# Kernel optimization log

Measured on AMD Instinct MI355X. Metric: run time of the kernel, lower is better.

Reference implementation:

```python
import jax, jax.numpy as jnp
import numpy as np

B, NQ, C = 2, 10000, 256
M, L, K = 8, 3, 4
D = C // M
LEVEL_SHAPES = [(100, 100), (50, 50), (25, 25)]


def setup_inputs() -> dict:
    key = jax.random.key(0)
    ks = jax.random.split(key, 16)
    inp = {
        "query": jax.random.normal(ks[0], (B, NQ, C), jnp.float32),
        "reference_points": jax.random.uniform(ks[1], (B, NQ, 2), jnp.float32),
        "value0": jax.random.normal(ks[2], (B, C) + LEVEL_SHAPES[0], jnp.float32),
        "value1": jax.random.normal(ks[3], (B, C) + LEVEL_SHAPES[1], jnp.float32),
        "value2": jax.random.normal(ks[4], (B, C) + LEVEL_SHAPES[2], jnp.float32),
        "Wv": jax.random.normal(ks[5], (C, C), jnp.float32) * 0.02,
        "bv": jnp.zeros((C,), jnp.float32),
        "Ws": jax.random.normal(ks[6], (M * L * K * 2, C), jnp.float32) * 0.05,
        "bs": jax.random.normal(ks[7], (M * L * K * 2,), jnp.float32),
        "Wa": jax.random.normal(ks[8], (M * L * K, C), jnp.float32) * 0.02,
        "ba": jnp.zeros((M * L * K,), jnp.float32),
        "Wo": jax.random.normal(ks[9], (C, C), jnp.float32) * 0.02,
        "bo": jnp.zeros((C,), jnp.float32),
    }
    return inp


def _bilinear_sample(vflat, px, py, H, W):
    """grid_sample bilinear, align_corners=False, padding_mode='zeros'.
    vflat: (B, M, H*W, D); px, py: (B, M, Q, K) pixel coords. -> (B, M, Q, K, D)
    """
    b, m, q, k = px.shape
    x0 = jnp.floor(px)
    y0 = jnp.floor(py)
    wx1 = px - x0  # frac weights (grad 1 w.r.t. px, matching grid_sample)
    wy1 = py - y0
    wx0 = 1.0 - wx1
    wy0 = 1.0 - wy1

    def gather(xi, yi):
        valid = ((xi >= 0) & (xi <= W - 1) & (yi >= 0) & (yi <= H - 1)).astype(vflat.dtype)
        xc = jnp.clip(xi, 0, W - 1).astype(jnp.int32)
        yc = jnp.clip(yi, 0, H - 1).astype(jnp.int32)
        idx = (yc * W + xc).reshape(b, m, q * k)
        g = jnp.take_along_axis(vflat, idx[..., None], axis=2)  # (B,M,QK,D)
        return g.reshape(b, m, q, k, -1) * valid[..., None]

    out = (gather(x0, y0) * (wx0 * wy0)[..., None]
           + gather(x0 + 1, y0) * (wx1 * wy0)[..., None]
           + gather(x0, y0 + 1) * (wx0 * wy1)[..., None]
           + gather(x0 + 1, y0 + 1) * (wx1 * wy1)[..., None])
    return out


def reference(query, reference_points, value0, value1, value2,
              Wv, bv, Ws, bs, Wa, ba, Wo, bo):
    bsz, nq, c = query.shape
    dt = query.dtype
    # sampling offsets and attention weights
    off = (query @ Ws.T + bs).reshape(bsz, nq, M, L, K, 2)
    attn = jax.nn.softmax((query @ Wa.T + ba).reshape(bsz, nq, M, L * K), axis=-1)
    attn = attn.reshape(bsz, nq, M, L, K)

    out = jnp.zeros((bsz, nq, M, D), dt)
    for li, v in enumerate([value0, value1, value2]):
        H, W = v.shape[2], v.shape[3]
        # conv1x1 value projection -> per-head maps (B, M, H*W, D)
        proj = jnp.einsum('bchw,oc->bohw', v, Wv) + bv[None, :, None, None]
        vflat = proj.reshape(bsz, M, D, H * W).transpose(0, 1, 3, 2)
        norm = jnp.asarray([W, H], dt)
        loc = reference_points[:, :, None, None, :] + off[:, :, :, li, :, :] / norm  # (B,Q,M,K,2)
        # grid = loc*2-1; pixel = (grid+1)*size/2 - 0.5 = loc*size - 0.5
        px = (loc[..., 0] * W - 0.5).transpose(0, 2, 1, 3)  # (B,M,Q,K)
        py = (loc[..., 1] * H - 0.5).transpose(0, 2, 1, 3)
        sampled = _bilinear_sample(vflat, px, py, H, W)  # (B,M,Q,K,D)
        out = out + jnp.einsum('bmqkd,bqmk->bqmd', sampled, attn[:, :, :, li, :])

    out = out.reshape(bsz, nq, c)
    return out @ Wo.T + bo
```

## Files before the change

### kernel.cpp

```cpp
#include <hip/hip_runtime.h>
#include <cstddef>

#define B_ 2
#define NQ_ 10000
#define C_ 256
#define M_ 8
#define L_ 3
#define K_ 4
#define D_ 32
#define P_ 13125

typedef unsigned short u16;
typedef __attribute__((ext_vector_type(8))) short short8;
typedef __attribute__((ext_vector_type(4))) float f32x4;

static __device__ __forceinline__ u16 f2bf(float f) {
    union { float f; unsigned u; } x; x.f = f;
    unsigned r = x.u + 0x7fffu + ((x.u >> 16) & 1u);
    return (u16)(r >> 16);
}
static __device__ __forceinline__ float bf2f(u16 u) {
    union { unsigned u; float f; } x; x.u = (unsigned)u << 16;
    return x.f;
}
static __device__ __forceinline__ short8 cvt8(const float4& a, const float4& b) {
    short8 r;
    r[0] = (short)f2bf(a.x); r[1] = (short)f2bf(a.y);
    r[2] = (short)f2bf(a.z); r[3] = (short)f2bf(a.w);
    r[4] = (short)f2bf(b.x); r[5] = (short)f2bf(b.y);
    r[6] = (short)f2bf(b.z); r[7] = (short)f2bf(b.w);
    return r;
}

__global__ __launch_bounds__(256) void transpose_value(
    const float* __restrict__ v0, const float* __restrict__ v1,
    const float* __restrict__ v2, u16* __restrict__ Vt)
{
    constexpr int HWs[3]  = {10000, 2500, 625};
    constexpr int offs[3] = {0, 10000, 12500};

    const int z   = blockIdx.z;
    const int b   = z / 3;
    const int lvl = z % 3;
    const int HW  = HWs[lvl];
    const int p0  = blockIdx.x * 64;
    if (p0 >= HW) return;
    const int c0  = blockIdx.y * 64;

    const float* V = (lvl == 0 ? v0 : (lvl == 1 ? v1 : v2)) + (size_t)b * 256 * HW;

    __shared__ u16 tile[64][66];
    const int t  = threadIdx.x;
    const int pl = t & 63;
    const int cb = t >> 6;

    #pragma unroll
    for (int i = 0; i < 16; ++i) {
        int c = cb + i * 4;
        float vv = 0.f;
        if (p0 + pl < HW)
            vv = V[(size_t)(c0 + c) * HW + p0 + pl];
        tile[pl][c] = f2bf(vv);
    }
    __syncthreads();

    const int cl = t & 63;
    const int pb = t >> 6;
    #pragma unroll
    for (int i = 0; i < 16; ++i) {
        int p = pb + i * 4;
        if (p0 + p < HW)
            Vt[((size_t)b * P_ + offs[lvl] + p0 + p) * 256 + c0 + cl] = tile[p][cl];
    }
}

template <bool AF32, typename OutT>
__global__ __launch_bounds__(256) void gemm_panel(
    const void* __restrict__ Av, int rows, int nRowTiles, int npanel,
    const float* __restrict__ B1f, const float* __restrict__ bias1, int N1,
    const float* __restrict__ B2f, const float* __restrict__ bias2, int Ntot,
    OutT* __restrict__ Cout)
{
    __shared__ u16 Bs[64 * 264];

    const int bid  = blockIdx.x;
    const int rlo  = bid & 7;
    const int tmp  = bid >> 3;
    const int panel = tmp % npanel;
    const int rowTile = (tmp / npanel) * 8 + rlo;
    if (rowTile >= nRowTiles) return;

    const int t  = threadIdx.x;
    const int w  = t >> 6;
    const int l  = t & 63;
    const int row0 = rowTile * 128 + w * 32;
    const int o0   = panel * 64;
    const int lr = l & 15;
    const int kb = (l >> 4) * 8;

    #pragma unroll
    for (int i = 0; i < 8; ++i) {
        int idx = i * 256 + t;
        int col = idx >> 5;
        int kc  = (idx & 31) * 8;
        int colg = min(o0 + col, Ntot - 1);
        const float* Br = ((colg < N1) ? B1f + (size_t)colg * 256
                                       : B2f + (size_t)(colg - N1) * 256) + kc;
        float4 f0 = *reinterpret_cast<const float4*>(Br);
        float4 f1 = *reinterpret_cast<const float4*>(Br + 4);
        *reinterpret_cast<short8*>(&Bs[col * 264 + kc]) = cvt8(f0, f1);
    }

    const int ra0 = min(row0 + lr,      rows - 1);
    const int ra1 = min(row0 + 16 + lr, rows - 1);

    __syncthreads();

    f32x4 acc[2][4] = {};

    if constexpr (AF32) {
        const float* Af  = (const float*)Av;
        const float* Ap0 = Af + (size_t)ra0 * 256 + kb;
        const float* Ap1 = Af + (size_t)ra1 * 256 + kb;
        #pragma unroll
        for (int k0 = 0; k0 < 256; k0 += 32) {
            float4 x0 = *reinterpret_cast<const float4*>(Ap0 + k0);
            float4 y0 = *reinterpret_cast<const float4*>(Ap0 + k0 + 4);
            float4 x1 = *reinterpret_cast<const float4*>(Ap1 + k0);
            float4 y1 = *reinterpret_cast<const float4*>(Ap1 + k0 + 4);
            short8 a0 = cvt8(x0, y0);
            short8 a1 = cvt8(x1, y1);
            short8 b0 = *reinterpret_cast<const short8*>(&Bs[(0 * 16 + lr) * 264 + kb + k0]);
            short8 b1 = *reinterpret_cast<const short8*>(&Bs[(1 * 16 + lr) * 264 + kb + k0]);
            short8 b2 = *reinterpret_cast<const short8*>(&Bs[(2 * 16 + lr) * 264 + kb + k0]);
            short8 b3 = *reinterpret_cast<const short8*>(&Bs[(3 * 16 + lr) * 264 + kb + k0]);
            acc[0][0] = __builtin_amdgcn_mfma_f32_16x16x32_bf16(a0, b0, acc[0][0], 0, 0, 0);
            acc[0][1] = __builtin_amdgcn_mfma_f32_16x16x32_bf16(a0, b1, acc[0][1], 0, 0, 0);
            acc[0][2] = __builtin_amdgcn_mfma_f32_16x16x32_bf16(a0, b2, acc[0][2], 0, 0, 0);
            acc[0][3] = __builtin_amdgcn_mfma_f32_16x16x32_bf16(a0, b3, acc[0][3], 0, 0, 0);
            acc[1][0] = __builtin_amdgcn_mfma_f32_16x16x32_bf16(a1, b0, acc[1][0], 0, 0, 0);
            acc[1][1] = __builtin_amdgcn_mfma_f32_16x16x32_bf16(a1, b1, acc[1][1], 0, 0, 0);
            acc[1][2] = __builtin_amdgcn_mfma_f32_16x16x32_bf16(a1, b2, acc[1][2], 0, 0, 0);
            acc[1][3] = __builtin_amdgcn_mfma_f32_16x16x32_bf16(a1, b3, acc[1][3], 0, 0, 0);
        }
    } else {
        const u16* Af  = (const u16*)Av;
        const u16* Ap0 = Af + (size_t)ra0 * 256 + kb;
        const u16* Ap1 = Af + (size_t)ra1 * 256 + kb;
        #pragma unroll
        for (int k0 = 0; k0 < 256; k0 += 32) {
            short8 a0 = *reinterpret_cast<const short8*>(Ap0 + k0);
            short8 a1 = *reinterpret_cast<const short8*>(Ap1 + k0);
            short8 b0 = *reinterpret_cast<const short8*>(&Bs[(0 * 16 + lr) * 264 + kb + k0]);
            short8 b1 = *reinterpret_cast<const short8*>(&Bs[(1 * 16 + lr) * 264 + kb + k0]);
            short8 b2 = *reinterpret_cast<const short8*>(&Bs[(2 * 16 + lr) * 264 + kb + k0]);
            short8 b3 = *reinterpret_cast<const short8*>(&Bs[(3 * 16 + lr) * 264 + kb + k0]);
            acc[0][0] = __builtin_amdgcn_mfma_f32_16x16x32_bf16(a0, b0, acc[0][0], 0, 0, 0);
            acc[0][1] = __builtin_amdgcn_mfma_f32_16x16x32_bf16(a0, b1, acc[0][1], 0, 0, 0);
            acc[0][2] = __builtin_amdgcn_mfma_f32_16x16x32_bf16(a0, b2, acc[0][2], 0, 0, 0);
            acc[0][3] = __builtin_amdgcn_mfma_f32_16x16x32_bf16(a0, b3, acc[0][3], 0, 0, 0);
            acc[1][0] = __builtin_amdgcn_mfma_f32_16x16x32_bf16(a1, b0, acc[1][0], 0, 0, 0);
            acc[1][1] = __builtin_amdgcn_mfma_f32_16x16x32_bf16(a1, b1, acc[1][1], 0, 0, 0);
            acc[1][2] = __builtin_amdgcn_mfma_f32_16x16x32_bf16(a1, b2, acc[1][2], 0, 0, 0);
            acc[1][3] = __builtin_amdgcn_mfma_f32_16x16x32_bf16(a1, b3, acc[1][3], 0, 0, 0);
        }
    }

    const int orow = (l >> 4) * 4;
    #pragma unroll
    for (int ct = 0; ct < 4; ++ct) {
        const int col = o0 + ct * 16 + lr;
        if (col >= Ntot) continue;
        const float bsv = (col < N1) ? bias1[col] : bias2[col - N1];
        #pragma unroll
        for (int rt = 0; rt < 2; ++rt) {
            #pragma unroll
            for (int r = 0; r < 4; ++r) {
                const int row = row0 + rt * 16 + orow + r;
                if (row < rows) {
                    float val = acc[rt][ct][r] + bsv;
                    if constexpr (sizeof(OutT) == 2)
                        Cout[(size_t)row * Ntot + col] = (OutT)f2bf(val);
                    else
                        Cout[(size_t)row * Ntot + col] = (OutT)val;
                }
            }
        }
    }
}

__global__ __launch_bounds__(256) void sample_kernel(
    const float* __restrict__ S,
    const float* __restrict__ refp,
    const u16* __restrict__ proj,
    u16* __restrict__ out2)
{
    constexpr int Wd[3]   = {100, 50, 25};
    constexpr int offs[3] = {0, 10000, 12500};

    __shared__ int   midx[192][4];
    __shared__ float mw[192][4];

    const int t = threadIdx.x;

    if (t < 192) {
        const int q  = t / 96;
        const int tq = t % 96;
        const int tm = tq / 12;
        const int tj = tq % 12;
        const int bq = blockIdx.x * 2 + q;
        const float* Sq = S + (size_t)bq * 288;

        float lg[12], mx = -1e30f;
        #pragma unroll
        for (int jj = 0; jj < 12; ++jj) {
            lg[jj] = Sq[192 + tm * 12 + jj];
            mx = fmaxf(mx, lg[jj]);
        }
        float sum = 0.f;
        #pragma unroll
        for (int jj = 0; jj < 12; ++jj) sum += __expf(lg[jj] - mx);
        const float attn = __expf(lg[tj] - mx) / sum;

        const int l  = tj >> 2;
        const int Wl = Wd[l];
        const float refx = refp[(size_t)bq * 2 + 0];
        const float refy = refp[(size_t)bq * 2 + 1];
        const float ox = Sq[(tm * 12 + tj) * 2 + 0];
        const float oy = Sq[(tm * 12 + tj) * 2 + 1];
        const float px = refx * (float)Wl + ox - 0.5f;
        const float py = refy * (float)Wl + oy - 0.5f;
        const float x0f = floorf(px), y0f = floorf(py);
        const float wx1 = px - x0f, wy1 = py - y0f;
        const float wx0 = 1.f - wx1, wy0 = 1.f - wy1;
        const int x0 = (int)x0f, y0 = (int)y0f;
        const int x1 = x0 + 1, y1 = y0 + 1;
        const bool vx0 = (unsigned)x0 < (unsigned)Wl;
        const bool vx1 = (unsigned)x1 < (unsigned)Wl;
        const bool vy0 = (unsigned)y0 < (unsigned)Wl;
        const bool vy1 = (unsigned)y1 < (unsigned)Wl;
        const int chb  = tm * 32;
        const int base = offs[l];
        midx[t][0] = (vx0 && vy0) ? ((base + y0 * Wl + x0) * 256 + chb) : 0;
        midx[t][1] = (vx1 && vy0) ? ((base + y0 * Wl + x1) * 256 + chb) : 0;
        midx[t][2] = (vx0 && vy1) ? ((base + y1 * Wl + x0) * 256 + chb) : 0;
        midx[t][3] = (vx1 && vy1) ? ((base + y1 * Wl + x1) * 256 + chb) : 0;
        mw[t][0] = (vx0 && vy0) ? attn * wx0 * wy0 : 0.f;
        mw[t][1] = (vx1 && vy0) ? attn * wx1 * wy0 : 0.f;
        mw[t][2] = (vx0 && vy1) ? attn * wx0 * wy1 : 0.f;
        mw[t][3] = (vx1 && vy1) ? attn * wx1 * wy1 : 0.f;
    }
    __syncthreads();

    const int qi  = t >> 7;
    const int tt  = t & 127;
    const int mh  = tt >> 4;
    const int d16 = tt & 15;
    const int bq2 = blockIdx.x * 2 + qi;
    const int b   = bq2 / NQ_;
    const u16* projb = proj + (size_t)b * P_ * 256 + 2 * d16;

    float acc0 = 0.f, acc1 = 0.f;

    #pragma unroll
    for (int j = 0; j < 12; ++j) {
        const int mj = qi * 96 + mh * 12 + j;
        const int4   o  = *reinterpret_cast<const int4*>(midx[mj]);
        const float4 ww = *reinterpret_cast<const float4*>(mw[mj]);
        const unsigned u00 = *reinterpret_cast<const unsigned*>(projb + o.x);
        const unsigned u10 = *reinterpret_cast<const unsigned*>(projb + o.y);
        const unsigned u01 = *reinterpret_cast<const unsigned*>(projb + o.z);
        const unsigned u11 = *reinterpret_cast<const unsigned*>(projb + o.w);
        union { unsigned u; float f; } c0, c1;
        c0.u = u00 << 16;          c1.u = u00 & 0xffff0000u;
        acc0 = fmaf(ww.x, c0.f, acc0); acc1 = fmaf(ww.x, c1.f, acc1);
        c0.u = u10 << 16;          c1.u = u10 & 0xffff0000u;
        acc0 = fmaf(ww.y, c0.f, acc0); acc1 = fmaf(ww.y, c1.f, acc1);
        c0.u = u01 << 16;          c1.u = u01 & 0xffff0000u;
        acc0 = fmaf(ww.z, c0.f, acc0); acc1 = fmaf(ww.z, c1.f, acc1);
        c0.u = u11 << 16;          c1.u = u11 & 0xffff0000u;
        acc0 = fmaf(ww.w, c0.f, acc0); acc1 = fmaf(ww.w, c1.f, acc1);
    }

    const unsigned packed = (unsigned)f2bf(acc0) | ((unsigned)f2bf(acc1) << 16);
    *reinterpret_cast<unsigned*>(out2 + (size_t)bq2 * 256 + mh * 32 + 2 * d16) = packed;
}

extern "C" void kernel_launch(void* const* d_in, const int* in_sizes, int n_in,
                              void* d_out, int out_size, void* d_ws, size_t ws_size,
                              hipStream_t stream)
{
    const float* query = (const float*)d_in[0];
    const float* refp  = (const float*)d_in[1];
    const float* v0    = (const float*)d_in[2];
    const float* v1    = (const float*)d_in[3];
    const float* v2    = (const float*)d_in[4];
    const float* Wv    = (const float*)d_in[5];
    const float* bv    = (const float*)d_in[6];
    const float* Ws    = (const float*)d_in[7];
    const float* bs    = (const float*)d_in[8];
    const float* Wa    = (const float*)d_in[9];
    const float* ba    = (const float*)d_in[10];
    const float* Wo    = (const float*)d_in[11];
    const float* bo    = (const float*)d_in[12];
    float* out = (float*)d_out;

    char* wsb = (char*)d_ws;
    u16*   proj  = (u16*)wsb;    wsb += (size_t)B_ * P_ * 256 * 2;
    float* S     = (float*)wsb;  wsb += (size_t)B_ * NQ_ * 288 * 4;
    u16*   Vt    = (u16*)wsb;    wsb += (size_t)B_ * P_ * 256 * 2;
    u16*   out2  = (u16*)wsb;    wsb += (size_t)B_ * NQ_ * 256 * 2;

    dim3 blk(256);

    transpose_value<<<dim3(157, 4, 6), blk, 0, stream>>>(v0, v1, v2, Vt);

    gemm_panel<false, u16><<<dim3(832), blk, 0, stream>>>(
        Vt, B_ * P_, 206, 4, Wv, bv, 256, Wv, bv, 256, proj);

    gemm_panel<true, float><<<dim3(800), blk, 0, stream>>>(
        query, B_ * NQ_, 157, 5, Ws, bs, 192, Wa, ba, 288, S);

    sample_kernel<<<dim3(NQ_), blk, 0, stream>>>(S, refp, proj, out2);

    gemm_panel<false, float><<<dim3(640), blk, 0, stream>>>(
        out2, B_ * NQ_, 157, 4, Wo, bo, 256, Wo, bo, 256, out);
}
```

Before: 202.5 us.

## Pre-convert query to bf16 and widen sampling kernel to four queries per block

Adds a standalone kernel that converts the fp32 query to bf16, so the offset/attention GEMM reads bf16 input instead of converting fp32 on the fly. The sampling kernel now handles four queries per block, with each thread loading four bf16 channels (8 bytes) per corner instead of two. It also software-pipelines the corner loads three steps ahead. This adds an extra kernel launch and a round trip of the query through memory, and increases register pressure in the sampler.

```diff
diff --git a/kernel.cpp b/kernel.cpp
--- a/kernel.cpp
+++ b/kernel.cpp
@@ -19,10 +19,6 @@
     unsigned r = x.u + 0x7fffu + ((x.u >> 16) & 1u);
     return (u16)(r >> 16);
 }
-static __device__ __forceinline__ float bf2f(u16 u) {
-    union { unsigned u; float f; } x; x.u = (unsigned)u << 16;
-    return x.f;
-}
 static __device__ __forceinline__ short8 cvt8(const float4& a, const float4& b) {
     short8 r;
     r[0] = (short)f2bf(a.x); r[1] = (short)f2bf(a.y);
@@ -30,6 +26,16 @@
     r[4] = (short)f2bf(b.x); r[5] = (short)f2bf(b.y);
     r[6] = (short)f2bf(b.z); r[7] = (short)f2bf(b.w);
     return r;
+}
+
+__global__ __launch_bounds__(256) void cvt_f32_bf16(
+    const float* __restrict__ in, u16* __restrict__ out, int n8)
+{
+    const int i = blockIdx.x * 256 + threadIdx.x;
+    if (i >= n8) return;
+    const float4 a = *reinterpret_cast<const float4*>(in + (size_t)i * 8);
+    const float4 b = *reinterpret_cast<const float4*>(in + (size_t)i * 8 + 4);
+    *reinterpret_cast<short8*>(out + (size_t)i * 8) = cvt8(a, b);
 }
 
 __global__ __launch_bounds__(256) void transpose_value(
@@ -198,17 +204,17 @@
     constexpr int Wd[3]   = {100, 50, 25};
     constexpr int offs[3] = {0, 10000, 12500};
 
-    __shared__ int   midx[192][4];
-    __shared__ float mw[192][4];
+    __shared__ int   midx[384][4];
+    __shared__ float mw[384][4];
 
     const int t = threadIdx.x;
 
-    if (t < 192) {
-        const int q  = t / 96;
-        const int tq = t % 96;
+    for (int job = t; job < 384; job += 256) {
+        const int q  = job / 96;
+        const int tq = job % 96;
         const int tm = tq / 12;
         const int tj = tq % 12;
-        const int bq = blockIdx.x * 2 + q;
+        const int bq = blockIdx.x * 4 + q;
         const float* Sq = S + (size_t)bq * 288;
 
         float lg[12], mx = -1e30f;
@@ -241,49 +247,71 @@
         const bool vy1 = (unsigned)y1 < (unsigned)Wl;
         const int chb  = tm * 32;
         const int base = offs[l];
-        midx[t][0] = (vx0 && vy0) ? ((base + y0 * Wl + x0) * 256 + chb) : 0;
-        midx[t][1] = (vx1 && vy0) ? ((base + y0 * Wl + x1) * 256 + chb) : 0;
-        midx[t][2] = (vx0 && vy1) ? ((base + y1 * Wl + x0) * 256 + chb) : 0;
-        midx[t][3] = (vx1 && vy1) ? ((base + y1 * Wl + x1) * 256 + chb) : 0;
-        mw[t][0] = (vx0 && vy0) ? attn * wx0 * wy0 : 0.f;
-        mw[t][1] = (vx1 && vy0) ? attn * wx1 * wy0 : 0.f;
-        mw[t][2] = (vx0 && vy1) ? attn * wx0 * wy1 : 0.f;
-        mw[t][3] = (vx1 && vy1) ? attn * wx1 * wy1 : 0.f;
+        midx[job][0] = (vx0 && vy0) ? ((base + y0 * Wl + x0) * 256 + chb) : 0;
+        midx[job][1] = (vx1 && vy0) ? ((base + y0 * Wl + x1) * 256 + chb) : 0;
+        midx[job][2] = (vx0 && vy1) ? ((base + y1 * Wl + x0) * 256 + chb) : 0;
+        midx[job][3] = (vx1 && vy1) ? ((base + y1 * Wl + x1) * 256 + chb) : 0;
+        mw[job][0] = (vx0 && vy0) ? attn * wx0 * wy0 : 0.f;
+        mw[job][1] = (vx1 && vy0) ? attn * wx1 * wy0 : 0.f;
+        mw[job][2] = (vx0 && vy1) ? attn * wx0 * wy1 : 0.f;
+        mw[job][3] = (vx1 && vy1) ? attn * wx1 * wy1 : 0.f;
     }
     __syncthreads();
 
-    const int qi  = t >> 7;
-    const int tt  = t & 127;
-    const int mh  = tt >> 4;
-    const int d16 = tt & 15;
-    const int bq2 = blockIdx.x * 2 + qi;
+    const int qi  = t >> 6;
+    const int tt  = t & 63;
+    const int mh  = tt >> 3;
+    const int d8  = tt & 7;
+    const int bq2 = blockIdx.x * 4 + qi;
     const int b   = bq2 / NQ_;
-    const u16* projb = proj + (size_t)b * P_ * 256 + 2 * d16;
-
-    float acc0 = 0.f, acc1 = 0.f;
+    const u16* projb = proj + (size_t)b * P_ * 256 + 4 * d8;
+    const int base_mj = qi * 96 + mh * 12;
+
+    float acc0 = 0.f, acc1 = 0.f, acc2 = 0.f, acc3 = 0.f;
+
+    uint2 v[4][4];
+    int4  o_[4];
+
+    #pragma unroll
+    for (int js = 0; js < 3; ++js) {
+        o_[js] = *reinterpret_cast<const int4*>(midx[base_mj + js]);
+        v[js][0] = *reinterpret_cast<const uint2*>(projb + o_[js].x);
+        v[js][1] = *reinterpret_cast<const uint2*>(projb + o_[js].y);
+        v[js][2] = *reinterpret_cast<const uint2*>(projb + o_[js].z);
+        v[js][3] = *reinterpret_cast<const uint2*>(projb + o_[js].w);
+    }
 
     #pragma unroll
     for (int j = 0; j < 12; ++j) {
-        const int mj = qi * 96 + mh * 12 + j;
-        const int4   o  = *reinterpret_cast<const int4*>(midx[mj]);
-        const float4 ww = *reinterpret_cast<const float4*>(mw[mj]);
-        const unsigned u00 = *reinterpret_cast<const unsigned*>(projb + o.x);
-        const unsigned u10 = *reinterpret_cast<const unsigned*>(projb + o.y);
-        const unsigned u01 = *reinterpret_cast<const unsigned*>(projb + o.z);
-        const unsigned u11 = *reinterpret_cast<const unsigned*>(projb + o.w);
-        union { unsigned u; float f; } c0, c1;
-        c0.u = u00 << 16;          c1.u = u00 & 0xffff0000u;
-        acc0 = fmaf(ww.x, c0.f, acc0); acc1 = fmaf(ww.x, c1.f, acc1);
-        c0.u = u10 << 16;          c1.u = u10 & 0xffff0000u;
-        acc0 = fmaf(ww.y, c0.f, acc0); acc1 = fmaf(ww.y, c1.f, acc1);
-        c0.u = u01 << 16;          c1.u = u01 & 0xffff0000u;
-        acc0 = fmaf(ww.z, c0.f, acc0); acc1 = fmaf(ww.z, c1.f, acc1);
-        c0.u = u11 << 16;          c1.u = u11 & 0xffff0000u;
-        acc0 = fmaf(ww.w, c0.f, acc0); acc1 = fmaf(ww.w, c1.f, acc1);
-    }
-
-    const unsigned packed = (unsigned)f2bf(acc0) | ((unsigned)f2bf(acc1) << 16);
-    *reinterpret_cast<unsigned*>(out2 + (size_t)bq2 * 256 + mh * 32 + 2 * d16) = packed;
+        const int s = j & 3;
+        if (j + 3 < 12) {
+            const int s3 = (j + 3) & 3;
+            o_[s3] = *reinterpret_cast<const int4*>(midx[base_mj + j + 3]);
+            v[s3][0] = *reinterpret_cast<const uint2*>(projb + o_[s3].x);
+            v[s3][1] = *reinterpret_cast<const uint2*>(projb + o_[s3].y);
+            v[s3][2] = *reinterpret_cast<const uint2*>(projb + o_[s3].z);
+            v[s3][3] = *reinterpret_cast<const uint2*>(projb + o_[s3].w);
+        }
+        const float4 ww = *reinterpret_cast<const float4*>(mw[base_mj + j]);
+        #pragma unroll
+        for (int c = 0; c < 4; ++c) {
+            const unsigned ux = v[s][c].x;
+            const unsigned uy = v[s][c].y;
+            const float wc = (c == 0) ? ww.x : (c == 1) ? ww.y : (c == 2) ? ww.z : ww.w;
+            union { unsigned u; float f; } e0, e1, e2, e3;
+            e0.u = ux << 16; e1.u = ux & 0xffff0000u;
+            e2.u = uy << 16; e3.u = uy & 0xffff0000u;
+            acc0 = fmaf(wc, e0.f, acc0);
+            acc1 = fmaf(wc, e1.f, acc1);
+            acc2 = fmaf(wc, e2.f, acc2);
+            acc3 = fmaf(wc, e3.f, acc3);
+        }
+    }
+
+    uint2 st;
+    st.x = (unsigned)f2bf(acc0) | ((unsigned)f2bf(acc1) << 16);
+    st.y = (unsigned)f2bf(acc2) | ((unsigned)f2bf(acc3) << 16);
+    *reinterpret_cast<uint2*>(out2 + (size_t)bq2 * 256 + mh * 32 + d8 * 4) = st;
 }
 
 extern "C" void kernel_launch(void* const* d_in, const int* in_sizes, int n_in,
@@ -310,18 +338,21 @@
     float* S     = (float*)wsb;  wsb += (size_t)B_ * NQ_ * 288 * 4;
     u16*   Vt    = (u16*)wsb;    wsb += (size_t)B_ * P_ * 256 * 2;
     u16*   out2  = (u16*)wsb;    wsb += (size_t)B_ * NQ_ * 256 * 2;
+    u16*   qbf   = (u16*)wsb;    wsb += (size_t)B_ * NQ_ * 256 * 2;
 
     dim3 blk(256);
+
+    cvt_f32_bf16<<<dim3(2500), blk, 0, stream>>>(query, qbf, 640000);
 
     transpose_value<<<dim3(157, 4, 6), blk, 0, stream>>>(v0, v1, v2, Vt);
 
     gemm_panel<false, u16><<<dim3(832), blk, 0, stream>>>(
         Vt, B_ * P_, 206, 4, Wv, bv, 256, Wv, bv, 256, proj);
 
-    gemm_panel<true, float><<<dim3(800), blk, 0, stream>>>(
-        query, B_ * NQ_, 157, 5, Ws, bs, 192, Wa, ba, 288, S);
-
-    sample_kernel<<<dim3(NQ_), blk, 0, stream>>>(S, refp, proj, out2);
+    gemm_panel<false, float><<<dim3(800), blk, 0, stream>>>(
+        qbf, B_ * NQ_, 157, 5, Ws, bs, 192, Wa, ba, 288, S);
+
+    sample_kernel<<<dim3(5000), blk, 0, stream>>>(S, refp, proj, out2);
 
     gemm_panel<false, float><<<dim3(640), blk, 0, stream>>>(
         out2, B_ * NQ_, 157, 4, Wo, bo, 256, Wo, bo, 256, out);
```

Measured after the change: 211.9 us. +4.6%, slower.
